# Performance work log

Hardware: AMD Instinct MI355X
Metric: run time of the kernel (lower is better)

Reference implementation:

```python
import jax, jax.numpy as jnp
import numpy as np

N_NODES = 25000
IN_DIM = 16
EDGE_DIM = 8
HID = 32
OUT_DIM = 16
N_EDGES = 400000
MLP_HID = 32


def setup_inputs() -> dict:
    key = jax.random.key(0)
    ks = jax.random.split(key, 12)
    x = jax.random.normal(ks[0], (N_NODES, IN_DIM), dtype=jnp.float32)
    edge_index = jax.random.randint(ks[1], (2, N_EDGES), 0, N_NODES, dtype=jnp.int32)
    edge_attr = jax.random.normal(ks[2], (N_EDGES, EDGE_DIM), dtype=jnp.float32)
    s = lambda fan_in: 1.0 / np.sqrt(fan_in)
    W1 = jax.random.uniform(ks[3], (EDGE_DIM, MLP_HID), minval=-s(EDGE_DIM), maxval=s(EDGE_DIM))
    b1 = jax.random.uniform(ks[4], (MLP_HID,), minval=-s(EDGE_DIM), maxval=s(EDGE_DIM))
    W2 = jax.random.uniform(ks[5], (MLP_HID, IN_DIM * HID), minval=-s(MLP_HID), maxval=s(MLP_HID))
    b2 = jax.random.uniform(ks[6], (IN_DIM * HID,), minval=-s(MLP_HID), maxval=s(MLP_HID))
    root = jax.random.uniform(ks[7], (IN_DIM, HID), minval=-s(IN_DIM), maxval=s(IN_DIM))
    bias = jnp.zeros((HID,), dtype=jnp.float32)
    Wlin = jax.random.uniform(ks[8], (HID, OUT_DIM), minval=-s(HID), maxval=s(HID))
    blin = jax.random.uniform(ks[9], (OUT_DIM,), minval=-s(HID), maxval=s(HID))
    return {"x": x, "edge_attr": edge_attr, "W1": W1, "b1": b1, "W2": W2,
            "b2": b2, "root": root, "bias": bias, "Wlin": Wlin, "blin": blin,
            "edge_index": edge_index}


def reference(x, edge_attr, W1, b1, W2, b2, root, bias, Wlin, blin, edge_index):
    src, dst = edge_index[0], edge_index[1]  # x_j gathered from src, aggregated at dst
    # edge MLP -> per-edge weight matrix [E, IN_DIM, HID]
    h = jax.nn.relu(edge_attr @ W1 + b1)
    W_e = (h @ W2 + b2).reshape(-1, IN_DIM, HID)
    # gather source features and per-edge matvec: [E, HID]
    msg = jnp.einsum('ei,eio->eo', x[src], W_e)
    # scatter-mean over target nodes
    agg = jax.ops.segment_sum(msg, dst, num_segments=N_NODES)
    cnt = jax.ops.segment_sum(jnp.ones((msg.shape[0],), dtype=msg.dtype), dst, num_segments=N_NODES)
    agg = agg / jnp.maximum(cnt, 1.0)[:, None]
    # NNConv root weight + bias, then ReLU and final linear
    out = jax.nn.relu(agg + x @ root + bias)
    return out @ Wlin + blin
```

## Files before the change

### kernel.cpp

```cpp
#include <hip/hip_runtime.h>
#include <cstdint>

#define E_EDGES 400000
#define N_NODES 25000
#define NU      12500
#define NPACK   18432
#define BLOCKS  1563
#define NWAVES  (BLOCKS*4)

typedef float f32x4 __attribute__((ext_vector_type(4)));
typedef __bf16 bf16x8 __attribute__((ext_vector_type(8)));

static __device__ __forceinline__ ushort f2bf(float f) {
    union { __bf16 b; ushort u; } c; c.b = (__bf16)f; return c.u;
}

__global__ void __launch_bounds__(256) k_pack(const float* __restrict__ W2,
                                              const float* __restrict__ b2,
                                              const float* __restrict__ W1,
                                              const int* __restrict__ ei,
                                              ushort* __restrict__ packed,
                                              uint* __restrict__ cnt_u) {
    int t = blockIdx.x * 256 + threadIdx.x;
    if (t < NPACK) {
        float v = 0.0f;
        if (t < 17408) {
            int j  = t & 7;
            int ln = (t >> 3) & 15;
            int kg = (t >> 7) & 3;
            int nt = (t >> 9) & 1;
            int kt = t >> 10;
            int kap = (j < 4) ? (kg * 4 + j) : (16 + kg * 4 + (j - 4));
            if (kt < 16)       v = W2[kap * 512 + kt * 32 + nt * 16 + ln];
            else if (kap < 16) v = b2[kap * 32 + nt * 16 + ln];
        } else {
            int idx  = t - 17408;
            int half = idx >> 9;
            int lane = (idx >> 3) & 63;
            int j    = idx & 7;
            int kg = lane >> 4, ln = lane & 15;
            if (kg == 0) v = W1[j * 32 + half * 16 + ln];
        }
        packed[t] = f2bf(v);
    }
    if (t < E_EDGES) atomicAdd(&cnt_u[ei[E_EDGES + t]], 1u);
}

__global__ void __launch_bounds__(256) k_edge(const float* __restrict__ ea,
                                              const float* __restrict__ x,
                                              const int* __restrict__ ei,
                                              const ushort* __restrict__ packed,
                                              const float* __restrict__ b1,
                                              float* __restrict__ agg) {
    __shared__ alignas(16) ushort w2l[NPACK];
    __shared__ float b1l[32];
    {
        const uint4* s = (const uint4*)packed;
        uint4* d = (uint4*)w2l;
        for (int i = threadIdx.x; i < NPACK / 8; i += 256) d[i] = s[i];
        if (threadIdx.x < 32) b1l[threadIdx.x] = b1[threadIdx.x];
    }
    __syncthreads();

    const int lane = threadIdx.x & 63;
    const int ln = lane & 15;
    const int kg = lane >> 4;
    const int wid = blockIdx.x * 4 + (threadIdx.x >> 6);

    const bf16x8 aw0 = *(const bf16x8*)(&w2l[17408 + lane * 8]);
    const bf16x8 aw1 = *(const bf16x8*)(&w2l[17408 + 512 + lane * 8]);
    const f32x4 z4 = {0.f, 0.f, 0.f, 0.f};
    const __bf16 zb = (__bf16)0.0f;

    int u = wid;
    int s0 = ei[u * 32 + ln];
    int s1 = ei[u * 32 + 16 + ln];
    int4 d0 = *(const int4*)(ei + E_EDGES + u * 32 + kg * 4);
    int4 d1 = *(const int4*)(ei + E_EDGES + u * 32 + 16 + kg * 4);
    const f32x4* ep0 = (const f32x4*)(ea + (size_t)(u * 32 + ln) * 8);
    f32x4 ea00 = ep0[0], ea01 = ep0[1];
    const f32x4* ep1 = (const f32x4*)(ea + (size_t)(u * 32 + 16 + ln) * 8);
    f32x4 ea10 = ep1[0], ea11 = ep1[1];

#pragma unroll
    for (int it = 0; it < 2; ++it) {
        const int un = u + NWAVES;
        const bool pf = (it == 0) && (un < NU);

        const f32x4* xp0 = (const f32x4*)(x + (size_t)s0 * 16);
        const f32x4 xa0 = xp0[0], xa1 = xp0[1], xa2 = xp0[2], xa3 = xp0[3];
        const f32x4* xp1 = (const f32x4*)(x + (size_t)s1 * 16);
        const f32x4 xb0 = xp1[0], xb1 = xp1[1], xb2 = xp1[2], xb3 = xp1[3];

        int ns0 = 0, ns1 = 0;
        int4 nd0 = {0,0,0,0}, nd1 = {0,0,0,0};
        f32x4 nea00 = z4, nea01 = z4, nea10 = z4, nea11 = z4;
        if (pf) {
            ns0 = ei[un * 32 + ln];
            ns1 = ei[un * 32 + 16 + ln];
            nd0 = *(const int4*)(ei + E_EDGES + un * 32 + kg * 4);
            nd1 = *(const int4*)(ei + E_EDGES + un * 32 + 16 + kg * 4);
            const f32x4* np0 = (const f32x4*)(ea + (size_t)(un * 32 + ln) * 8);
            nea00 = np0[0]; nea01 = np0[1];
            const f32x4* np1 = (const f32x4*)(ea + (size_t)(un * 32 + 16 + ln) * 8);
            nea10 = np1[0]; nea11 = np1[1];
        }

        bf16x8 eb0, eb1;
        if (kg == 0) {
            eb0[0]=(__bf16)ea00[0]; eb0[1]=(__bf16)ea00[1]; eb0[2]=(__bf16)ea00[2]; eb0[3]=(__bf16)ea00[3];
            eb0[4]=(__bf16)ea01[0]; eb0[5]=(__bf16)ea01[1]; eb0[6]=(__bf16)ea01[2]; eb0[7]=(__bf16)ea01[3];
            eb1[0]=(__bf16)ea10[0]; eb1[1]=(__bf16)ea10[1]; eb1[2]=(__bf16)ea10[2]; eb1[3]=(__bf16)ea10[3];
            eb1[4]=(__bf16)ea11[0]; eb1[5]=(__bf16)ea11[1]; eb1[6]=(__bf16)ea11[2]; eb1[7]=(__bf16)ea11[3];
        } else {
            eb0[0]=zb; eb0[1]=zb; eb0[2]=zb; eb0[3]=zb; eb0[4]=zb; eb0[5]=zb; eb0[6]=zb; eb0[7]=zb;
            eb1 = eb0;
        }
        f32x4 hA0 = __builtin_amdgcn_mfma_f32_16x16x32_bf16(aw0, eb0, z4, 0, 0, 0);
        f32x4 hA1 = __builtin_amdgcn_mfma_f32_16x16x32_bf16(aw1, eb0, z4, 0, 0, 0);
        f32x4 hB0 = __builtin_amdgcn_mfma_f32_16x16x32_bf16(aw0, eb1, z4, 0, 0, 0);
        f32x4 hB1 = __builtin_amdgcn_mfma_f32_16x16x32_bf16(aw1, eb1, z4, 0, 0, 0);

        float h0[8], h1[8];
#pragma unroll
        for (int r = 0; r < 4; ++r) {
            const float blo = b1l[4 * kg + r], bhi = b1l[16 + 4 * kg + r];
            h0[r]     = fmaxf(hA0[r] + blo, 0.f);
            h0[4 + r] = fmaxf(hA1[r] + bhi, 0.f);
            h1[r]     = fmaxf(hB0[r] + blo, 0.f);
            h1[4 + r] = fmaxf(hB1[r] + bhi, 0.f);
        }

        float xr0[16], xr1[16];
        xr0[0]=xa0[0]; xr0[1]=xa0[1]; xr0[2]=xa0[2]; xr0[3]=xa0[3];
        xr0[4]=xa1[0]; xr0[5]=xa1[1]; xr0[6]=xa1[2]; xr0[7]=xa1[3];
        xr0[8]=xa2[0]; xr0[9]=xa2[1]; xr0[10]=xa2[2]; xr0[11]=xa2[3];
        xr0[12]=xa3[0]; xr0[13]=xa3[1]; xr0[14]=xa3[2]; xr0[15]=xa3[3];
        xr1[0]=xb0[0]; xr1[1]=xb0[1]; xr1[2]=xb0[2]; xr1[3]=xb0[3];
        xr1[4]=xb1[0]; xr1[5]=xb1[1]; xr1[6]=xb1[2]; xr1[7]=xb1[3];
        xr1[8]=xb2[0]; xr1[9]=xb2[1]; xr1[10]=xb2[2]; xr1[11]=xb2[3];
        xr1[12]=xb3[0]; xr1[13]=xb3[1]; xr1[14]=xb3[2]; xr1[15]=xb3[3];

        f32x4 acc00 = z4, acc01 = z4, acc10 = z4, acc11 = z4;

#pragma unroll
        for (int kt = 0; kt < 16; ++kt) {
            const bf16x8 bf0 = *(const bf16x8*)(&w2l[(kt * 2 + 0) * 512 + lane * 8]);
            const bf16x8 bf1 = *(const bf16x8*)(&w2l[(kt * 2 + 1) * 512 + lane * 8]);
            const float xv0 = xr0[kt], xv1 = xr1[kt];
            bf16x8 a0, a1;
#pragma unroll
            for (int j = 0; j < 8; ++j) {
                a0[j] = (__bf16)(xv0 * h0[j]);
                a1[j] = (__bf16)(xv1 * h1[j]);
            }
            acc00 = __builtin_amdgcn_mfma_f32_16x16x32_bf16(a0, bf0, acc00, 0, 0, 0);
            acc10 = __builtin_amdgcn_mfma_f32_16x16x32_bf16(a1, bf0, acc10, 0, 0, 0);
            acc01 = __builtin_amdgcn_mfma_f32_16x16x32_bf16(a0, bf1, acc01, 0, 0, 0);
            acc11 = __builtin_amdgcn_mfma_f32_16x16x32_bf16(a1, bf1, acc11, 0, 0, 0);
        }
        {
            const f32x4 xs0 = (kg == 0) ? xa0 : ((kg == 1) ? xa1 : ((kg == 2) ? xa2 : xa3));
            const f32x4 xs1 = (kg == 0) ? xb0 : ((kg == 1) ? xb1 : ((kg == 2) ? xb2 : xb3));
            bf16x8 a0, a1;
            a0[0]=(__bf16)xs0[0]; a0[1]=(__bf16)xs0[1]; a0[2]=(__bf16)xs0[2]; a0[3]=(__bf16)xs0[3];
            a0[4]=zb; a0[5]=zb; a0[6]=zb; a0[7]=zb;
            a1[0]=(__bf16)xs1[0]; a1[1]=(__bf16)xs1[1]; a1[2]=(__bf16)xs1[2]; a1[3]=(__bf16)xs1[3];
            a1[4]=zb; a1[5]=zb; a1[6]=zb; a1[7]=zb;
            const bf16x8 bf0 = *(const bf16x8*)(&w2l[(16 * 2 + 0) * 512 + lane * 8]);
            const bf16x8 bf1 = *(const bf16x8*)(&w2l[(16 * 2 + 1) * 512 + lane * 8]);
            acc00 = __builtin_amdgcn_mfma_f32_16x16x32_bf16(a0, bf0, acc00, 0, 0, 0);
            acc10 = __builtin_amdgcn_mfma_f32_16x16x32_bf16(a1, bf0, acc10, 0, 0, 0);
            acc01 = __builtin_amdgcn_mfma_f32_16x16x32_bf16(a0, bf1, acc01, 0, 0, 0);
            acc11 = __builtin_amdgcn_mfma_f32_16x16x32_bf16(a1, bf1, acc11, 0, 0, 0);
        }

        atomicAdd(&agg[d0.x * 32 + ln],      acc00[0]);
        atomicAdd(&agg[d0.y * 32 + ln],      acc00[1]);
        atomicAdd(&agg[d0.z * 32 + ln],      acc00[2]);
        atomicAdd(&agg[d0.w * 32 + ln],      acc00[3]);
        atomicAdd(&agg[d0.x * 32 + 16 + ln], acc01[0]);
        atomicAdd(&agg[d0.y * 32 + 16 + ln], acc01[1]);
        atomicAdd(&agg[d0.z * 32 + 16 + ln], acc01[2]);
        atomicAdd(&agg[d0.w * 32 + 16 + ln], acc01[3]);
        atomicAdd(&agg[d1.x * 32 + ln],      acc10[0]);
        atomicAdd(&agg[d1.y * 32 + ln],      acc10[1]);
        atomicAdd(&agg[d1.z * 32 + ln],      acc10[2]);
        atomicAdd(&agg[d1.w * 32 + ln],      acc10[3]);
        atomicAdd(&agg[d1.x * 32 + 16 + ln], acc11[0]);
        atomicAdd(&agg[d1.y * 32 + 16 + ln], acc11[1]);
        atomicAdd(&agg[d1.z * 32 + 16 + ln], acc11[2]);
        atomicAdd(&agg[d1.w * 32 + 16 + ln], acc11[3]);

        if (!pf) break;
        u = un;
        s0 = ns0; s1 = ns1; d0 = nd0; d1 = nd1;
        ea00 = nea00; ea01 = nea01; ea10 = nea10; ea11 = nea11;
    }
}

__global__ void __launch_bounds__(256) k_node(const float* __restrict__ agg,
                                              const uint* __restrict__ cnt_u,
                                              const float* __restrict__ x,
                                              const float* __restrict__ root,
                                              const float* __restrict__ bias,
                                              const float* __restrict__ Wlin,
                                              const float* __restrict__ blin,
                                              float* __restrict__ out) {
    __shared__ float al[256];
    const int n0 = blockIdx.x * 8;
    const int t = threadIdx.x;
    const int n = n0 + (t >> 5), h = t & 31;
    float a = 0.0f;
    if (n < N_NODES) {
        const float c = (float)cnt_u[n];
        float s = agg[n * 32 + h] / fmaxf(c, 1.0f) + bias[h];
        const f32x4* xp = (const f32x4*)(x + (size_t)n * 16);
        const f32x4 x0 = xp[0], x1 = xp[1], x2 = xp[2], x3 = xp[3];
        float xv[16];
        xv[0]=x0[0]; xv[1]=x0[1]; xv[2]=x0[2]; xv[3]=x0[3];
        xv[4]=x1[0]; xv[5]=x1[1]; xv[6]=x1[2]; xv[7]=x1[3];
        xv[8]=x2[0]; xv[9]=x2[1]; xv[10]=x2[2]; xv[11]=x2[3];
        xv[12]=x3[0]; xv[13]=x3[1]; xv[14]=x3[2]; xv[15]=x3[3];
#pragma unroll
        for (int i = 0; i < 16; ++i) s += xv[i] * root[i * 32 + h];
        a = fmaxf(s, 0.0f);
    }
    al[t] = a;
    __syncthreads();
    if (t < 128) {
        const int nj = n0 + (t >> 4), j = t & 15;
        if (nj < N_NODES) {
            float s = blin[j];
#pragma unroll
            for (int h2 = 0; h2 < 32; ++h2) s += al[(t >> 4) * 32 + h2] * Wlin[h2 * 16 + j];
            out[nj * 16 + j] = s;
        }
    }
}

extern "C" void kernel_launch(void* const* d_in, const int* in_sizes, int n_in,
                              void* d_out, int out_size, void* d_ws, size_t ws_size,
                              hipStream_t stream) {
    const float* x    = (const float*)d_in[0];
    const float* ea   = (const float*)d_in[1];
    const float* W1   = (const float*)d_in[2];
    const float* b1   = (const float*)d_in[3];
    const float* W2   = (const float*)d_in[4];
    const float* b2   = (const float*)d_in[5];
    const float* root = (const float*)d_in[6];
    const float* bias = (const float*)d_in[7];
    const float* Wlin = (const float*)d_in[8];
    const float* blin = (const float*)d_in[9];
    const int*   ei   = (const int*)d_in[10];
    float* out = (float*)d_out;

    char* ws = (char*)d_ws;
    float*  agg    = (float*)(ws + 0);
    uint*   cnt_u  = (uint*)(ws + 3200000);
    ushort* packed = (ushort*)(ws + 3300000);

    hipMemsetAsync(d_ws, 0, 3300000, stream);

    k_pack<<<BLOCKS, 256, 0, stream>>>(W2, b2, W1, ei, packed, cnt_u);
    k_edge<<<BLOCKS, 256, 0, stream>>>(ea, x, ei, packed, b1, agg);
    k_node<<<3125, 256, 0, stream>>>(agg, cnt_u, x, root, bias, Wlin, blin, out);
}
```

Before: 90.29 us.

## Hold packed W2 fragments in registers and run a persistent edge loop

The edge kernel no longer stages the packed W2/b2 weights in shared memory. Each lane instead loads all 34 bf16x8 weight fragments into registers once, and b1 is read as vectors. Each wave now handles 16 edges per step inside a grid-stride loop over half as many blocks. The next group's x gather is software-prefetched in the middle of the MFMA chain. This removes the per-block LDS fill, the barrier and the LDS reads in the inner loop, in exchange for much higher register pressure (136 VGPRs of weights) and a possible occupancy drop.

After: 87.18 us. -3.4%, faster.

```diff
diff --git a/kernel.cpp b/kernel.cpp
--- a/kernel.cpp
+++ b/kernel.cpp
@@ -3,10 +3,10 @@
 
 #define E_EDGES 400000
 #define N_NODES 25000
-#define NU      12500
+#define NG      25000
 #define NPACK   18432
-#define BLOCKS  1563
-#define NWAVES  (BLOCKS*4)
+#define EBLOCKS 782
+#define NWAVES_E (EBLOCKS*4)
 
 typedef float f32x4 __attribute__((ext_vector_type(4)));
 typedef __bf16 bf16x8 __attribute__((ext_vector_type(8)));
@@ -46,156 +46,124 @@
     if (t < E_EDGES) atomicAdd(&cnt_u[ei[E_EDGES + t]], 1u);
 }
 
-__global__ void __launch_bounds__(256) k_edge(const float* __restrict__ ea,
-                                              const float* __restrict__ x,
-                                              const int* __restrict__ ei,
-                                              const ushort* __restrict__ packed,
-                                              const float* __restrict__ b1,
-                                              float* __restrict__ agg) {
-    __shared__ alignas(16) ushort w2l[NPACK];
-    __shared__ float b1l[32];
-    {
-        const uint4* s = (const uint4*)packed;
-        uint4* d = (uint4*)w2l;
-        for (int i = threadIdx.x; i < NPACK / 8; i += 256) d[i] = s[i];
-        if (threadIdx.x < 32) b1l[threadIdx.x] = b1[threadIdx.x];
-    }
-    __syncthreads();
-
+__global__ void __launch_bounds__(256, 2) k_edge(const float* __restrict__ ea,
+                                                 const float* __restrict__ x,
+                                                 const int* __restrict__ ei,
+                                                 const ushort* __restrict__ packed,
+                                                 const float* __restrict__ b1,
+                                                 float* __restrict__ agg) {
     const int lane = threadIdx.x & 63;
     const int ln = lane & 15;
     const int kg = lane >> 4;
     const int wid = blockIdx.x * 4 + (threadIdx.x >> 6);
 
-    const bf16x8 aw0 = *(const bf16x8*)(&w2l[17408 + lane * 8]);
-    const bf16x8 aw1 = *(const bf16x8*)(&w2l[17408 + 512 + lane * 8]);
+    bf16x8 wfr[34];
+#pragma unroll
+    for (int i = 0; i < 34; ++i)
+        wfr[i] = *(const bf16x8*)(packed + (size_t)i * 512 + (size_t)lane * 8);
+    const bf16x8 aw0 = *(const bf16x8*)(packed + 17408 + (size_t)lane * 8);
+    const bf16x8 aw1 = *(const bf16x8*)(packed + 17408 + 512 + (size_t)lane * 8);
+    const f32x4 blo4 = *(const f32x4*)(b1 + 4 * kg);
+    const f32x4 bhi4 = *(const f32x4*)(b1 + 16 + 4 * kg);
+
     const f32x4 z4 = {0.f, 0.f, 0.f, 0.f};
     const __bf16 zb = (__bf16)0.0f;
 
-    int u = wid;
-    int s0 = ei[u * 32 + ln];
-    int s1 = ei[u * 32 + 16 + ln];
-    int4 d0 = *(const int4*)(ei + E_EDGES + u * 32 + kg * 4);
-    int4 d1 = *(const int4*)(ei + E_EDGES + u * 32 + 16 + kg * 4);
-    const f32x4* ep0 = (const f32x4*)(ea + (size_t)(u * 32 + ln) * 8);
-    f32x4 ea00 = ep0[0], ea01 = ep0[1];
-    const f32x4* ep1 = (const f32x4*)(ea + (size_t)(u * 32 + 16 + ln) * 8);
-    f32x4 ea10 = ep1[0], ea11 = ep1[1];
-
-#pragma unroll
-    for (int it = 0; it < 2; ++it) {
-        const int un = u + NWAVES;
-        const bool pf = (it == 0) && (un < NU);
-
-        const f32x4* xp0 = (const f32x4*)(x + (size_t)s0 * 16);
-        const f32x4 xa0 = xp0[0], xa1 = xp0[1], xa2 = xp0[2], xa3 = xp0[3];
-        const f32x4* xp1 = (const f32x4*)(x + (size_t)s1 * 16);
-        const f32x4 xb0 = xp1[0], xb1 = xp1[1], xb2 = xp1[2], xb3 = xp1[3];
-
-        int ns0 = 0, ns1 = 0;
-        int4 nd0 = {0,0,0,0}, nd1 = {0,0,0,0};
-        f32x4 nea00 = z4, nea01 = z4, nea10 = z4, nea11 = z4;
+    int g = wid;
+    f32x4 ea0, ea1, xq0, xq1, xq2, xq3;
+    {
+        const int s0 = ei[g * 16 + ln];
+        const f32x4* ep = (const f32x4*)(ea + (size_t)(g * 16 + ln) * 8);
+        ea0 = ep[0]; ea1 = ep[1];
+        const f32x4* xp = (const f32x4*)(x + (size_t)s0 * 16);
+        xq0 = xp[0]; xq1 = xp[1]; xq2 = xp[2]; xq3 = xp[3];
+    }
+
+    while (true) {
+        const int gn = g + NWAVES_E;
+        const bool pf = gn < NG;
+
+        int ns0 = 0;
+        f32x4 nea0 = z4, nea1 = z4;
         if (pf) {
-            ns0 = ei[un * 32 + ln];
-            ns1 = ei[un * 32 + 16 + ln];
-            nd0 = *(const int4*)(ei + E_EDGES + un * 32 + kg * 4);
-            nd1 = *(const int4*)(ei + E_EDGES + un * 32 + 16 + kg * 4);
-            const f32x4* np0 = (const f32x4*)(ea + (size_t)(un * 32 + ln) * 8);
-            nea00 = np0[0]; nea01 = np0[1];
-            const f32x4* np1 = (const f32x4*)(ea + (size_t)(un * 32 + 16 + ln) * 8);
-            nea10 = np1[0]; nea11 = np1[1];
-        }
-
-        bf16x8 eb0, eb1;
+            ns0 = ei[gn * 16 + ln];
+            const f32x4* nep = (const f32x4*)(ea + (size_t)(gn * 16 + ln) * 8);
+            nea0 = nep[0]; nea1 = nep[1];
+        }
+        const int4 d4 = *(const int4*)(ei + E_EDGES + g * 16 + kg * 4);
+
+        bf16x8 eb;
         if (kg == 0) {
-            eb0[0]=(__bf16)ea00[0]; eb0[1]=(__bf16)ea00[1]; eb0[2]=(__bf16)ea00[2]; eb0[3]=(__bf16)ea00[3];
-            eb0[4]=(__bf16)ea01[0]; eb0[5]=(__bf16)ea01[1]; eb0[6]=(__bf16)ea01[2]; eb0[7]=(__bf16)ea01[3];
-            eb1[0]=(__bf16)ea10[0]; eb1[1]=(__bf16)ea10[1]; eb1[2]=(__bf16)ea10[2]; eb1[3]=(__bf16)ea10[3];
-            eb1[4]=(__bf16)ea11[0]; eb1[5]=(__bf16)ea11[1]; eb1[6]=(__bf16)ea11[2]; eb1[7]=(__bf16)ea11[3];
+            eb[0]=(__bf16)ea0[0]; eb[1]=(__bf16)ea0[1]; eb[2]=(__bf16)ea0[2]; eb[3]=(__bf16)ea0[3];
+            eb[4]=(__bf16)ea1[0]; eb[5]=(__bf16)ea1[1]; eb[6]=(__bf16)ea1[2]; eb[7]=(__bf16)ea1[3];
         } else {
-            eb0[0]=zb; eb0[1]=zb; eb0[2]=zb; eb0[3]=zb; eb0[4]=zb; eb0[5]=zb; eb0[6]=zb; eb0[7]=zb;
-            eb1 = eb0;
-        }
-        f32x4 hA0 = __builtin_amdgcn_mfma_f32_16x16x32_bf16(aw0, eb0, z4, 0, 0, 0);
-        f32x4 hA1 = __builtin_amdgcn_mfma_f32_16x16x32_bf16(aw1, eb0, z4, 0, 0, 0);
-        f32x4 hB0 = __builtin_amdgcn_mfma_f32_16x16x32_bf16(aw0, eb1, z4, 0, 0, 0);
-        f32x4 hB1 = __builtin_amdgcn_mfma_f32_16x16x32_bf16(aw1, eb1, z4, 0, 0, 0);
-
-        float h0[8], h1[8];
+            eb[0]=zb; eb[1]=zb; eb[2]=zb; eb[3]=zb; eb[4]=zb; eb[5]=zb; eb[6]=zb; eb[7]=zb;
+        }
+        const f32x4 hA0 = __builtin_amdgcn_mfma_f32_16x16x32_bf16(aw0, eb, z4, 0, 0, 0);
+        const f32x4 hA1 = __builtin_amdgcn_mfma_f32_16x16x32_bf16(aw1, eb, z4, 0, 0, 0);
+
+        float h[8];
 #pragma unroll
         for (int r = 0; r < 4; ++r) {
-            const float blo = b1l[4 * kg + r], bhi = b1l[16 + 4 * kg + r];
-            h0[r]     = fmaxf(hA0[r] + blo, 0.f);
-            h0[4 + r] = fmaxf(hA1[r] + bhi, 0.f);
-            h1[r]     = fmaxf(hB0[r] + blo, 0.f);
-            h1[4 + r] = fmaxf(hB1[r] + bhi, 0.f);
-        }
-
-        float xr0[16], xr1[16];
-        xr0[0]=xa0[0]; xr0[1]=xa0[1]; xr0[2]=xa0[2]; xr0[3]=xa0[3];
-        xr0[4]=xa1[0]; xr0[5]=xa1[1]; xr0[6]=xa1[2]; xr0[7]=xa1[3];
-        xr0[8]=xa2[0]; xr0[9]=xa2[1]; xr0[10]=xa2[2]; xr0[11]=xa2[3];
-        xr0[12]=xa3[0]; xr0[13]=xa3[1]; xr0[14]=xa3[2]; xr0[15]=xa3[3];
-        xr1[0]=xb0[0]; xr1[1]=xb0[1]; xr1[2]=xb0[2]; xr1[3]=xb0[3];
-        xr1[4]=xb1[0]; xr1[5]=xb1[1]; xr1[6]=xb1[2]; xr1[7]=xb1[3];
-        xr1[8]=xb2[0]; xr1[9]=xb2[1]; xr1[10]=xb2[2]; xr1[11]=xb2[3];
-        xr1[12]=xb3[0]; xr1[13]=xb3[1]; xr1[14]=xb3[2]; xr1[15]=xb3[3];
-
-        f32x4 acc00 = z4, acc01 = z4, acc10 = z4, acc11 = z4;
-
-#pragma unroll
-        for (int kt = 0; kt < 16; ++kt) {
-            const bf16x8 bf0 = *(const bf16x8*)(&w2l[(kt * 2 + 0) * 512 + lane * 8]);
-            const bf16x8 bf1 = *(const bf16x8*)(&w2l[(kt * 2 + 1) * 512 + lane * 8]);
-            const float xv0 = xr0[kt], xv1 = xr1[kt];
-            bf16x8 a0, a1;
-#pragma unroll
-            for (int j = 0; j < 8; ++j) {
-                a0[j] = (__bf16)(xv0 * h0[j]);
-                a1[j] = (__bf16)(xv1 * h1[j]);
-            }
-            acc00 = __builtin_amdgcn_mfma_f32_16x16x32_bf16(a0, bf0, acc00, 0, 0, 0);
-            acc10 = __builtin_amdgcn_mfma_f32_16x16x32_bf16(a1, bf0, acc10, 0, 0, 0);
-            acc01 = __builtin_amdgcn_mfma_f32_16x16x32_bf16(a0, bf1, acc01, 0, 0, 0);
-            acc11 = __builtin_amdgcn_mfma_f32_16x16x32_bf16(a1, bf1, acc11, 0, 0, 0);
+            h[r]     = fmaxf(hA0[r] + blo4[r], 0.f);
+            h[4 + r] = fmaxf(hA1[r] + bhi4[r], 0.f);
+        }
+
+        float xr[16];
+        xr[0]=xq0[0]; xr[1]=xq0[1]; xr[2]=xq0[2]; xr[3]=xq0[3];
+        xr[4]=xq1[0]; xr[5]=xq1[1]; xr[6]=xq1[2]; xr[7]=xq1[3];
+        xr[8]=xq2[0]; xr[9]=xq2[1]; xr[10]=xq2[2]; xr[11]=xq2[3];
+        xr[12]=xq3[0]; xr[13]=xq3[1]; xr[14]=xq3[2]; xr[15]=xq3[3];
+
+        f32x4 acc0 = z4, acc1 = z4;
+
+#pragma unroll
+        for (int kt = 0; kt < 8; ++kt) {
+            const float xv = xr[kt];
+            bf16x8 a;
+#pragma unroll
+            for (int j = 0; j < 8; ++j) a[j] = (__bf16)(xv * h[j]);
+            acc0 = __builtin_amdgcn_mfma_f32_16x16x32_bf16(a, wfr[kt * 2 + 0], acc0, 0, 0, 0);
+            acc1 = __builtin_amdgcn_mfma_f32_16x16x32_bf16(a, wfr[kt * 2 + 1], acc1, 0, 0, 0);
+        }
+
+        f32x4 nx0 = z4, nx1 = z4, nx2 = z4, nx3 = z4;
+        if (pf) {
+            const f32x4* nxp = (const f32x4*)(x + (size_t)ns0 * 16);
+            nx0 = nxp[0]; nx1 = nxp[1]; nx2 = nxp[2]; nx3 = nxp[3];
+        }
+
+#pragma unroll
+        for (int kt = 8; kt < 16; ++kt) {
+            const float xv = xr[kt];
+            bf16x8 a;
+#pragma unroll
+            for (int j = 0; j < 8; ++j) a[j] = (__bf16)(xv * h[j]);
+            acc0 = __builtin_amdgcn_mfma_f32_16x16x32_bf16(a, wfr[kt * 2 + 0], acc0, 0, 0, 0);
+            acc1 = __builtin_amdgcn_mfma_f32_16x16x32_bf16(a, wfr[kt * 2 + 1], acc1, 0, 0, 0);
         }
         {
-            const f32x4 xs0 = (kg == 0) ? xa0 : ((kg == 1) ? xa1 : ((kg == 2) ? xa2 : xa3));
-            const f32x4 xs1 = (kg == 0) ? xb0 : ((kg == 1) ? xb1 : ((kg == 2) ? xb2 : xb3));
-            bf16x8 a0, a1;
-            a0[0]=(__bf16)xs0[0]; a0[1]=(__bf16)xs0[1]; a0[2]=(__bf16)xs0[2]; a0[3]=(__bf16)xs0[3];
-            a0[4]=zb; a0[5]=zb; a0[6]=zb; a0[7]=zb;
-            a1[0]=(__bf16)xs1[0]; a1[1]=(__bf16)xs1[1]; a1[2]=(__bf16)xs1[2]; a1[3]=(__bf16)xs1[3];
-            a1[4]=zb; a1[5]=zb; a1[6]=zb; a1[7]=zb;
-            const bf16x8 bf0 = *(const bf16x8*)(&w2l[(16 * 2 + 0) * 512 + lane * 8]);
-            const bf16x8 bf1 = *(const bf16x8*)(&w2l[(16 * 2 + 1) * 512 + lane * 8]);
-            acc00 = __builtin_amdgcn_mfma_f32_16x16x32_bf16(a0, bf0, acc00, 0, 0, 0);
-            acc10 = __builtin_amdgcn_mfma_f32_16x16x32_bf16(a1, bf0, acc10, 0, 0, 0);
-            acc01 = __builtin_amdgcn_mfma_f32_16x16x32_bf16(a0, bf1, acc01, 0, 0, 0);
-            acc11 = __builtin_amdgcn_mfma_f32_16x16x32_bf16(a1, bf1, acc11, 0, 0, 0);
-        }
-
-        atomicAdd(&agg[d0.x * 32 + ln],      acc00[0]);
-        atomicAdd(&agg[d0.y * 32 + ln],      acc00[1]);
-        atomicAdd(&agg[d0.z * 32 + ln],      acc00[2]);
-        atomicAdd(&agg[d0.w * 32 + ln],      acc00[3]);
-        atomicAdd(&agg[d0.x * 32 + 16 + ln], acc01[0]);
-        atomicAdd(&agg[d0.y * 32 + 16 + ln], acc01[1]);
-        atomicAdd(&agg[d0.z * 32 + 16 + ln], acc01[2]);
-        atomicAdd(&agg[d0.w * 32 + 16 + ln], acc01[3]);
-        atomicAdd(&agg[d1.x * 32 + ln],      acc10[0]);
-        atomicAdd(&agg[d1.y * 32 + ln],      acc10[1]);
-        atomicAdd(&agg[d1.z * 32 + ln],      acc10[2]);
-        atomicAdd(&agg[d1.w * 32 + ln],      acc10[3]);
-        atomicAdd(&agg[d1.x * 32 + 16 + ln], acc11[0]);
-        atomicAdd(&agg[d1.y * 32 + 16 + ln], acc11[1]);
-        atomicAdd(&agg[d1.z * 32 + 16 + ln], acc11[2]);
-        atomicAdd(&agg[d1.w * 32 + 16 + ln], acc11[3]);
+            const f32x4 xs = (kg == 0) ? xq0 : ((kg == 1) ? xq1 : ((kg == 2) ? xq2 : xq3));
+            bf16x8 a;
+            a[0]=(__bf16)xs[0]; a[1]=(__bf16)xs[1]; a[2]=(__bf16)xs[2]; a[3]=(__bf16)xs[3];
+            a[4]=zb; a[5]=zb; a[6]=zb; a[7]=zb;
+            acc0 = __builtin_amdgcn_mfma_f32_16x16x32_bf16(a, wfr[32], acc0, 0, 0, 0);
+            acc1 = __builtin_amdgcn_mfma_f32_16x16x32_bf16(a, wfr[33], acc1, 0, 0, 0);
+        }
+
+        atomicAdd(&agg[d4.x * 32 + ln],      acc0[0]);
+        atomicAdd(&agg[d4.y * 32 + ln],      acc0[1]);
+        atomicAdd(&agg[d4.z * 32 + ln],      acc0[2]);
+        atomicAdd(&agg[d4.w * 32 + ln],      acc0[3]);
+        atomicAdd(&agg[d4.x * 32 + 16 + ln], acc1[0]);
+        atomicAdd(&agg[d4.y * 32 + 16 + ln], acc1[1]);
+        atomicAdd(&agg[d4.z * 32 + 16 + ln], acc1[2]);
+        atomicAdd(&agg[d4.w * 32 + 16 + ln], acc1[3]);
 
         if (!pf) break;
-        u = un;
-        s0 = ns0; s1 = ns1; d0 = nd0; d1 = nd1;
-        ea00 = nea00; ea01 = nea01; ea10 = nea10; ea11 = nea11;
+        g = gn;
+        ea0 = nea0; ea1 = nea1;
+        xq0 = nx0; xq1 = nx1; xq2 = nx2; xq3 = nx3;
     }
 }
 
@@ -262,7 +230,7 @@
 
     hipMemsetAsync(d_ws, 0, 3300000, stream);
 
-    k_pack<<<BLOCKS, 256, 0, stream>>>(W2, b2, W1, ei, packed, cnt_u);
-    k_edge<<<BLOCKS, 256, 0, stream>>>(ea, x, ei, packed, b1, agg);
+    k_pack<<<1563, 256, 0, stream>>>(W2, b2, W1, ei, packed, cnt_u);
+    k_edge<<<EBLOCKS, 256, 0, stream>>>(ea, x, ei, packed, b1, agg);
     k_node<<<3125, 256, 0, stream>>>(agg, cnt_u, x, root, bias, Wlin, blin, out);
 }
```

## Fuse workspace zeroing into pack kernel, move degree counting into edge kernel

Applied to the files above, without the earlier changes.

Replaces the memset with a grid-stride zeroing loop inside the pack kernel and moves the per-destination degree atomics into the edge kernel. The edge kernel becomes a persistent grid-stride loop over 1024 blocks with prefetch. It reads W1 weights and b1 straight from global instead of staging them in LDS, shrinking shared memory. It also raises wave priority around the MFMA loop. This removes one launch and a separate atomic pass, at the cost of extra atomics in the hot kernel and fewer blocks.

After: 83.41 us. 1.08x faster.

```diff
diff --git a/kernel.cpp b/kernel.cpp
--- a/kernel.cpp
+++ b/kernel.cpp
@@ -5,45 +5,43 @@
 #define N_NODES 25000
 #define NU      12500
 #define NPACK   18432
-#define BLOCKS  1563
-#define NWAVES  (BLOCKS*4)
-
-typedef float f32x4 __attribute__((ext_vector_type(4)));
+#define EBLOCKS 1024
+#define ESTRIDE (EBLOCKS*4)
+
+typedef float  f32x4  __attribute__((ext_vector_type(4)));
 typedef __bf16 bf16x8 __attribute__((ext_vector_type(8)));
 
 static __device__ __forceinline__ ushort f2bf(float f) {
     union { __bf16 b; ushort u; } c; c.b = (__bf16)f; return c.u;
 }
 
-__global__ void __launch_bounds__(256) k_pack(const float* __restrict__ W2,
-                                              const float* __restrict__ b2,
-                                              const float* __restrict__ W1,
-                                              const int* __restrict__ ei,
-                                              ushort* __restrict__ packed,
-                                              uint* __restrict__ cnt_u) {
-    int t = blockIdx.x * 256 + threadIdx.x;
-    if (t < NPACK) {
-        float v = 0.0f;
-        if (t < 17408) {
-            int j  = t & 7;
-            int ln = (t >> 3) & 15;
-            int kg = (t >> 7) & 3;
-            int nt = (t >> 9) & 1;
-            int kt = t >> 10;
-            int kap = (j < 4) ? (kg * 4 + j) : (16 + kg * 4 + (j - 4));
-            if (kt < 16)       v = W2[kap * 512 + kt * 32 + nt * 16 + ln];
-            else if (kap < 16) v = b2[kap * 32 + nt * 16 + ln];
-        } else {
-            int idx  = t - 17408;
-            int half = idx >> 9;
-            int lane = (idx >> 3) & 63;
-            int j    = idx & 7;
-            int kg = lane >> 4, ln = lane & 15;
-            if (kg == 0) v = W1[j * 32 + half * 16 + ln];
-        }
-        packed[t] = f2bf(v);
-    }
-    if (t < E_EDGES) atomicAdd(&cnt_u[ei[E_EDGES + t]], 1u);
+__global__ void __launch_bounds__(256) k_pre(const float* __restrict__ W2,
+                                             const float* __restrict__ b2,
+                                             const float* __restrict__ W1,
+                                             ushort* __restrict__ packed,
+                                             uint* __restrict__ zbase) {
+    const int t = blockIdx.x * 256 + threadIdx.x;
+    for (int i = t; i < 825000; i += EBLOCKS * 256) zbase[i] = 0u;
+    if (t >= NPACK) return;
+    float v = 0.0f;
+    if (t < 17408) {
+        int j  = t & 7;
+        int ln = (t >> 3) & 15;
+        int kg = (t >> 7) & 3;
+        int nt = (t >> 9) & 1;
+        int kt = t >> 10;
+        int kap = (j < 4) ? (kg * 4 + j) : (16 + kg * 4 + (j - 4));
+        if (kt < 16)       v = W2[kap * 512 + kt * 32 + nt * 16 + ln];
+        else if (kap < 16) v = b2[kap * 32 + nt * 16 + ln];
+    } else {
+        int idx  = t - 17408;
+        int half = idx >> 9;
+        int lane = (idx >> 3) & 63;
+        int j    = idx & 7;
+        int kg = lane >> 4, ln = lane & 15;
+        if (kg == 0) v = W1[j * 32 + half * 16 + ln];
+    }
+    packed[t] = f2bf(v);
 }
 
 __global__ void __launch_bounds__(256) k_edge(const float* __restrict__ ea,
@@ -51,14 +49,13 @@
                                               const int* __restrict__ ei,
                                               const ushort* __restrict__ packed,
                                               const float* __restrict__ b1,
-                                              float* __restrict__ agg) {
-    __shared__ alignas(16) ushort w2l[NPACK];
-    __shared__ float b1l[32];
+                                              float* __restrict__ agg,
+                                              uint* __restrict__ cnt_u) {
+    __shared__ alignas(16) ushort w2l[17408];
     {
         const uint4* s = (const uint4*)packed;
         uint4* d = (uint4*)w2l;
-        for (int i = threadIdx.x; i < NPACK / 8; i += 256) d[i] = s[i];
-        if (threadIdx.x < 32) b1l[threadIdx.x] = b1[threadIdx.x];
+        for (int i = threadIdx.x; i < 2176; i += 256) d[i] = s[i];
     }
     __syncthreads();
 
@@ -67,8 +64,11 @@
     const int kg = lane >> 4;
     const int wid = blockIdx.x * 4 + (threadIdx.x >> 6);
 
-    const bf16x8 aw0 = *(const bf16x8*)(&w2l[17408 + lane * 8]);
-    const bf16x8 aw1 = *(const bf16x8*)(&w2l[17408 + 512 + lane * 8]);
+    const bf16x8 aw0 = *(const bf16x8*)(packed + 17408 + (size_t)lane * 8);
+    const bf16x8 aw1 = *(const bf16x8*)(packed + 17408 + 512 + (size_t)lane * 8);
+    const f32x4 blo4 = *(const f32x4*)(b1 + 4 * kg);
+    const f32x4 bhi4 = *(const f32x4*)(b1 + 16 + 4 * kg);
+
     const f32x4 z4 = {0.f, 0.f, 0.f, 0.f};
     const __bf16 zb = (__bf16)0.0f;
 
@@ -77,20 +77,29 @@
     int s1 = ei[u * 32 + 16 + ln];
     int4 d0 = *(const int4*)(ei + E_EDGES + u * 32 + kg * 4);
     int4 d1 = *(const int4*)(ei + E_EDGES + u * 32 + 16 + kg * 4);
-    const f32x4* ep0 = (const f32x4*)(ea + (size_t)(u * 32 + ln) * 8);
-    f32x4 ea00 = ep0[0], ea01 = ep0[1];
-    const f32x4* ep1 = (const f32x4*)(ea + (size_t)(u * 32 + 16 + ln) * 8);
-    f32x4 ea10 = ep1[0], ea11 = ep1[1];
-
-#pragma unroll
-    for (int it = 0; it < 2; ++it) {
-        const int un = u + NWAVES;
-        const bool pf = (it == 0) && (un < NU);
+    f32x4 ea00, ea01, ea10, ea11;
+    {
+        const f32x4* ep0 = (const f32x4*)(ea + (size_t)(u * 32 + ln) * 8);
+        ea00 = ep0[0]; ea01 = ep0[1];
+        const f32x4* ep1 = (const f32x4*)(ea + (size_t)(u * 32 + 16 + ln) * 8);
+        ea10 = ep1[0]; ea11 = ep1[1];
+    }
+
+    while (true) {
+        const int un = u + ESTRIDE;
+        const bool pf = un < NU;
 
         const f32x4* xp0 = (const f32x4*)(x + (size_t)s0 * 16);
         const f32x4 xa0 = xp0[0], xa1 = xp0[1], xa2 = xp0[2], xa3 = xp0[3];
         const f32x4* xp1 = (const f32x4*)(x + (size_t)s1 * 16);
         const f32x4 xb0 = xp1[0], xb1 = xp1[1], xb2 = xp1[2], xb3 = xp1[3];
+
+        if (ln < 4) {
+            const int dA = (ln == 0) ? d0.x : ((ln == 1) ? d0.y : ((ln == 2) ? d0.z : d0.w));
+            const int dB = (ln == 0) ? d1.x : ((ln == 1) ? d1.y : ((ln == 2) ? d1.z : d1.w));
+            atomicAdd(&cnt_u[dA], 1u);
+            atomicAdd(&cnt_u[dB], 1u);
+        }
 
         int ns0 = 0, ns1 = 0;
         int4 nd0 = {0,0,0,0}, nd1 = {0,0,0,0};
@@ -116,15 +125,15 @@
             eb0[0]=zb; eb0[1]=zb; eb0[2]=zb; eb0[3]=zb; eb0[4]=zb; eb0[5]=zb; eb0[6]=zb; eb0[7]=zb;
             eb1 = eb0;
         }
-        f32x4 hA0 = __builtin_amdgcn_mfma_f32_16x16x32_bf16(aw0, eb0, z4, 0, 0, 0);
-        f32x4 hA1 = __builtin_amdgcn_mfma_f32_16x16x32_bf16(aw1, eb0, z4, 0, 0, 0);
-        f32x4 hB0 = __builtin_amdgcn_mfma_f32_16x16x32_bf16(aw0, eb1, z4, 0, 0, 0);
-        f32x4 hB1 = __builtin_amdgcn_mfma_f32_16x16x32_bf16(aw1, eb1, z4, 0, 0, 0);
+        const f32x4 hA0 = __builtin_amdgcn_mfma_f32_16x16x32_bf16(aw0, eb0, z4, 0, 0, 0);
+        const f32x4 hA1 = __builtin_amdgcn_mfma_f32_16x16x32_bf16(aw1, eb0, z4, 0, 0, 0);
+        const f32x4 hB0 = __builtin_amdgcn_mfma_f32_16x16x32_bf16(aw0, eb1, z4, 0, 0, 0);
+        const f32x4 hB1 = __builtin_amdgcn_mfma_f32_16x16x32_bf16(aw1, eb1, z4, 0, 0, 0);
 
         float h0[8], h1[8];
 #pragma unroll
         for (int r = 0; r < 4; ++r) {
-            const float blo = b1l[4 * kg + r], bhi = b1l[16 + 4 * kg + r];
+            const float blo = blo4[r], bhi = bhi4[r];
             h0[r]     = fmaxf(hA0[r] + blo, 0.f);
             h0[4 + r] = fmaxf(hA1[r] + bhi, 0.f);
             h1[r]     = fmaxf(hB0[r] + blo, 0.f);
@@ -143,6 +152,7 @@
 
         f32x4 acc00 = z4, acc01 = z4, acc10 = z4, acc11 = z4;
 
+        __builtin_amdgcn_s_setprio(1);
 #pragma unroll
         for (int kt = 0; kt < 16; ++kt) {
             const bf16x8 bf0 = *(const bf16x8*)(&w2l[(kt * 2 + 0) * 512 + lane * 8]);
@@ -174,6 +184,7 @@
             acc01 = __builtin_amdgcn_mfma_f32_16x16x32_bf16(a0, bf1, acc01, 0, 0, 0);
             acc11 = __builtin_amdgcn_mfma_f32_16x16x32_bf16(a1, bf1, acc11, 0, 0, 0);
         }
+        __builtin_amdgcn_s_setprio(0);
 
         atomicAdd(&agg[d0.x * 32 + ln],      acc00[0]);
         atomicAdd(&agg[d0.y * 32 + ln],      acc00[1]);
@@ -260,9 +271,7 @@
     uint*   cnt_u  = (uint*)(ws + 3200000);
     ushort* packed = (ushort*)(ws + 3300000);
 
-    hipMemsetAsync(d_ws, 0, 3300000, stream);
-
-    k_pack<<<BLOCKS, 256, 0, stream>>>(W2, b2, W1, ei, packed, cnt_u);
-    k_edge<<<BLOCKS, 256, 0, stream>>>(ea, x, ei, packed, b1, agg);
+    k_pre<<<EBLOCKS, 256, 0, stream>>>(W2, b2, W1, packed, (uint*)ws);
+    k_edge<<<EBLOCKS, 256, 0, stream>>>(ea, x, ei, packed, b1, agg, cnt_u);
     k_node<<<3125, 256, 0, stream>>>(agg, cnt_u, x, root, bias, Wlin, blin, out);
 }
```
